# Optimization experiments

Hardware: AMD Instinct MI355X
Metric: run time of the kernel (lower is better)

Reference implementation:

```python
import jax, jax.numpy as jnp
import numpy as np

DIM = 512
HEADS = 8
HEAD_DIM = DIM // HEADS
SCALING = float(np.sqrt(HEAD_DIM))
B, S = 8, 2048


def setup_inputs() -> dict:
    key = jax.random.key(0)
    ks = jax.random.split(key, 6)
    x = jax.random.normal(ks[0], (B, S, DIM), dtype=jnp.float32)
    mask = jax.random.randint(ks[1], (B, S), 0, 2).astype(bool)
    mask = mask.at[:, 0].set(False)  # guarantee at least one unmasked key per row
    lim_qkv = 1.0 / np.sqrt(DIM)
    Wqkv = jax.random.uniform(ks[2], (3 * DIM, DIM), minval=-lim_qkv, maxval=lim_qkv, dtype=jnp.float32)
    bqkv = jax.random.uniform(ks[3], (3 * DIM,), minval=-lim_qkv, maxval=lim_qkv, dtype=jnp.float32)
    Wout = jax.random.uniform(ks[4], (DIM, DIM), minval=-lim_qkv, maxval=lim_qkv, dtype=jnp.float32)
    bout = jax.random.uniform(ks[5], (DIM,), minval=-lim_qkv, maxval=lim_qkv, dtype=jnp.float32)
    ln_g = jnp.ones((DIM,), dtype=jnp.float32)
    ln_b = jnp.zeros((DIM,), dtype=jnp.float32)
    return {"x": x, "mask": mask, "Wqkv": Wqkv, "bqkv": bqkv, "Wout": Wout, "bout": bout, "ln_g": ln_g, "ln_b": ln_b}


def reference(x, mask, Wqkv, bqkv, Wout, bout, ln_g, ln_b):
    b, s, _ = x.shape
    qkv = x @ Wqkv.T + bqkv                                   # [b, s, 3*dim]
    qkv = qkv.reshape(b, s, HEADS, HEAD_DIM, 3)               # torch reshape semantics (interleaved)
    q = qkv[..., 0]                                           # [b, s, h, d]
    k = qkv[..., 1]
    v = jax.nn.elu(qkv[..., 2])
    attn = jnp.einsum('bqhd,bkhd->bhqk', q, k) / SCALING      # [b, h, s, s]
    bias = jnp.where(mask[:, None, None, :], -jnp.inf, 0.0).astype(attn.dtype)
    attn = jax.nn.softmax(attn + bias, axis=-1)
    out = jnp.einsum('bhqk,bkhd->bqhd', attn, v).reshape(b, s, DIM)
    out = out @ Wout.T + bout
    mu = jnp.mean(out, axis=-1, keepdims=True)
    var = jnp.var(out, axis=-1, keepdims=True)
    out = (out - mu) / jnp.sqrt(var + 1e-5) * ln_g + ln_b
    return jax.nn.elu(out)
```

## Files before the change

### kernel.cpp

```cpp
#include <hip/hip_runtime.h>

#define DIM 512
#define HEADS 8
#define HD 64
#define NB 8
#define NS 2048
#define SCALE_INV 0.125f
#define C2F 0.18033688011112042f
#define NEG_BIG -1e30f
#define QSZ 8388608

typedef __attribute__((ext_vector_type(8))) short bf16x8;
typedef __attribute__((ext_vector_type(4))) float f32x4;

__device__ __forceinline__ float elu_f(float x) {
    return x > 0.0f ? x : (__expf(x) - 1.0f);
}
__device__ __forceinline__ short f2bf(float x) {
    union { float f; unsigned u; } v; v.f = x;
    unsigned r = v.u + 0x7FFFu + ((v.u >> 16) & 1u);
    return (short)(r >> 16);
}
__device__ __forceinline__ float exp2_hw(float x) {
    float r; asm("v_exp_f32 %0, %1" : "=v"(r) : "v"(x)); return r;
}
__device__ __forceinline__ unsigned cvt_pk_bf16(float a, float b) {
    unsigned r; asm("v_cvt_pk_bf16_f32 %0, %1, %2" : "=v"(r) : "v"(a), "v"(b)); return r;
}

__device__ __forceinline__ void gload16(const void* g, void* l) {
    __builtin_amdgcn_global_load_lds(
        (const __attribute__((address_space(1))) unsigned*)g,
        (__attribute__((address_space(3))) unsigned*)l, 16, 0, 0);
}
__device__ __forceinline__ void gload4(const void* g, void* l) {
    __builtin_amdgcn_global_load_lds(
        (const __attribute__((address_space(1))) unsigned*)g,
        (__attribute__((address_space(3))) unsigned*)l, 4, 0, 0);
}

#define X4 2097152
#define W14 196608
#define W24 65536
__global__ __launch_bounds__(256) void prep(
    const float* __restrict__ x, const float* __restrict__ Wqkv,
    const float* __restrict__ bqkv, const float* __restrict__ Wout,
    const int* __restrict__ mask,
    short* __restrict__ xb, short* __restrict__ Wp,
    float* __restrict__ bp, short* __restrict__ Wob,
    float* __restrict__ maskf)
{
    int i = blockIdx.x * 256 + threadIdx.x;
    if (i < X4) {
        float4 v = *(const float4*)(x + (size_t)i * 4);
        ushort4 o; o.x = (unsigned short)f2bf(v.x); o.y = (unsigned short)f2bf(v.y);
        o.z = (unsigned short)f2bf(v.z); o.w = (unsigned short)f2bf(v.w);
        *(ushort4*)(xb + (size_t)i * 4) = o;
    } else if (i < X4 + W14) {
        int j = i - X4;
        int np = j >> 7, k = (j & 127) * 4;
        int w = np >> 9, h = (np >> 6) & 7, d = np & 63;
        int n = h * 192 + d * 3 + w;
        float4 v = *(const float4*)(Wqkv + (size_t)n * 512 + k);
        ushort4 o; o.x = (unsigned short)f2bf(v.x); o.y = (unsigned short)f2bf(v.y);
        o.z = (unsigned short)f2bf(v.z); o.w = (unsigned short)f2bf(v.w);
        *(ushort4*)(Wp + (size_t)np * 512 + k) = o;
    } else if (i < X4 + W14 + W24) {
        int j = i - X4 - W14;
        float4 v = *(const float4*)(Wout + (size_t)j * 4);
        ushort4 o; o.x = (unsigned short)f2bf(v.x); o.y = (unsigned short)f2bf(v.y);
        o.z = (unsigned short)f2bf(v.z); o.w = (unsigned short)f2bf(v.w);
        *(ushort4*)(Wob + (size_t)j * 4) = o;
    } else if (i < X4 + W14 + W24 + 1536) {
        int j = i - X4 - W14 - W24;
        int w = j >> 9, h = (j >> 6) & 7, d = j & 63;
        bp[j] = bqkv[h * 192 + d * 3 + w];
    } else {
        int j = i - X4 - W14 - W24 - 1536;
        maskf[j] = mask[j] ? NEG_BIG : 0.0f;
    }
}

__global__ __launch_bounds__(256) void qkv_mfma(
    const short* __restrict__ A, const short* __restrict__ Bw,
    const float* __restrict__ bp, short* __restrict__ QKV)
{
    __shared__ short smem[2 * 128 * 64];
    short* As = smem;
    short* Bs = smem + 128 * 64;
    const int t = threadIdx.x, lane = t & 63, wv = t >> 6;
    const int c = lane & 15, quad = lane >> 4;
    const int wr = wv >> 1, wc = wv & 1;
    const int rsub = lane >> 3;
    const int csA = (lane & 7) ^ rsub;
    const int m0 = blockIdx.x * 128, n0 = blockIdx.y * 128;
    f32x4 acc[4][4];
    #pragma unroll
    for (int mi = 0; mi < 4; ++mi)
        #pragma unroll
        for (int nj = 0; nj < 4; ++nj)
            #pragma unroll
            for (int i = 0; i < 4; ++i) acc[mi][nj][i] = 0.0f;

    for (int k0 = 0; k0 < 512; k0 += 64) {
        if (k0) __syncthreads();
        #pragma unroll
        for (int p = 0; p < 4; ++p) {
            int r = p * 32 + wv * 8 + rsub;
            gload16(A  + (size_t)(m0 + r) * 512 + k0 + csA * 8, &As[(p * 4 + wv) * 512]);
            gload16(Bw + (size_t)(n0 + r) * 512 + k0 + csA * 8, &Bs[(p * 4 + wv) * 512]);
        }
        __syncthreads();
        bf16x8 af[4][2], bfr[4][2];
        #pragma unroll
        for (int mi = 0; mi < 4; ++mi) {
            int ar = wr * 64 + mi * 16 + c;
            af[mi][0] = *(const bf16x8*)&As[ar * 64 + ((quad       ^ (ar & 7)) * 8)];
            af[mi][1] = *(const bf16x8*)&As[ar * 64 + (((4 + quad) ^ (ar & 7)) * 8)];
        }
        #pragma unroll
        for (int nj = 0; nj < 4; ++nj) {
            int br = wc * 64 + nj * 16 + c;
            bfr[nj][0] = *(const bf16x8*)&Bs[br * 64 + ((quad       ^ (br & 7)) * 8)];
            bfr[nj][1] = *(const bf16x8*)&Bs[br * 64 + (((4 + quad) ^ (br & 7)) * 8)];
        }
        __builtin_amdgcn_s_setprio(1);
        #pragma unroll
        for (int mi = 0; mi < 4; ++mi)
            #pragma unroll
            for (int nj = 0; nj < 4; ++nj) {
                acc[mi][nj] = __builtin_amdgcn_mfma_f32_16x16x32_bf16(af[mi][0], bfr[nj][0], acc[mi][nj], 0, 0, 0);
                acc[mi][nj] = __builtin_amdgcn_mfma_f32_16x16x32_bf16(af[mi][1], bfr[nj][1], acc[mi][nj], 0, 0, 0);
            }
        __builtin_amdgcn_s_setprio(0);
    }

    const int w  = n0 >> 9;
    const int b  = m0 >> 11;
    const int hh = ((n0 + wc * 64) >> 6) & 7;
    float bv[4];
    #pragma unroll
    for (int nj = 0; nj < 4; ++nj) bv[nj] = bp[n0 + wc * 64 + nj * 16 + c];

    if (w < 2) {
        short* out = QKV + (size_t)w * QSZ + (size_t)(b * 8 + hh) * NS * 64;
        #pragma unroll
        for (int mi = 0; mi < 4; ++mi)
            #pragma unroll
            for (int i = 0; i < 4; ++i) {
                int s = (m0 & (NS - 1)) + wr * 64 + mi * 16 + quad * 4 + i;
                #pragma unroll
                for (int nj = 0; nj < 4; ++nj)
                    out[(size_t)s * 64 + nj * 16 + c] = f2bf(acc[mi][nj][i] + bv[nj]);
            }
    } else {
        __syncthreads();
        short* T = smem;
        #pragma unroll
        for (int mi = 0; mi < 4; ++mi)
            #pragma unroll
            for (int i = 0; i < 4; ++i) {
                int ml = wr * 64 + mi * 16 + quad * 4 + i;
                int mb = ml >> 3, mr = ml & 7;
                #pragma unroll
                for (int nj = 0; nj < 4; ++nj) {
                    int nl = wc * 64 + nj * 16 + c;
                    T[nl * 128 + ((mb ^ (nl & 15)) * 8) + mr] =
                        f2bf(elu_f(acc[mi][nj][i] + bv[nj]));
                }
            }
        __syncthreads();
        short* Vt = QKV + (size_t)2 * QSZ;
        #pragma unroll
        for (int p = 0; p < 8; ++p) {
            int idx = p * 256 + t, row = idx >> 4, ch = idx & 15;
            uint4 v = *(const uint4*)&T[row * 128 + ((ch ^ (row & 15)) * 8)];
            int d = row & 63;
            int h2 = ((n0 + row) >> 6) & 7;
            int sg = (m0 & (NS - 1)) + ch * 8;
            int kt = sg >> 6, ks = sg & 63;
            *(uint4*)(Vt + (((size_t)(b * 8 + h2) * 32 + kt) * 64 + d) * 64 + ks) = v;
        }
    }
}

__global__ __launch_bounds__(512, 4) void attn_mfma(
    const short* __restrict__ Qg, const short* __restrict__ Kg,
    const short* __restrict__ Vg, const float* __restrict__ maskf,
    short* __restrict__ O)
{
    __shared__ short Pt[128 * 64];
    __shared__ short Ks[2][64 * 64];
    __shared__ short Vs[2][64 * 64];
    __shared__ float msk[2][64];
    __shared__ float lw[128];

    const int t = threadIdx.x;
    const int lane = t & 63;
    const int wv = t >> 6;
    const int wq = wv & 3;
    const int wk = wv >> 2;
    const int c = lane & 15;
    const int quad = lane >> 4;
    const int bid = blockIdx.x;
    const int qt = bid & 15;
    const int h  = (bid >> 4) & 7;
    const int b  = bid >> 7;
    const int g  = b * 8 + h;
    const size_t base = (size_t)g * NS * HD;
    const int q0 = qt * 128;

    const int rsub = lane >> 3;
    const int csA  = (lane & 7) ^ rsub;
    const int csV  = ((lane & 7) - rsub) & 7;

    #pragma unroll
    for (int p = 0; p < 2; ++p) {
        int r = wv * 16 + p * 8 + rsub;
        gload16(Qg + base + (size_t)(q0 + r) * HD + csA * 8, &Pt[(wv * 2 + p) * 512]);
    }
    {
        int r = wv * 8 + rsub;
        gload16(Kg + base + (size_t)r * HD + csA * 8, &Ks[0][wv * 512]);
        gload16(Vg + (((size_t)g * 32 + 0) * 64 + r) * 64 + csV * 8, &Vs[0][wv * 512]);
        if (wv == 0) gload4(maskf + (size_t)b * NS + lane, &msk[0][0]);
    }
    __syncthreads();

    bf16x8 bq[2][2];
    #pragma unroll
    for (int nj = 0; nj < 2; ++nj) {
        int mq = wq * 32 + nj * 16 + c;
        bq[nj][0] = *(const bf16x8*)&Pt[mq * 64 + ((quad       ^ (mq & 7)) * 8)];
        bq[nj][1] = *(const bf16x8*)&Pt[mq * 64 + (((4 + quad) ^ (mq & 7)) * 8)];
    }
    __syncthreads();

    {
        int r = wv * 8 + rsub;
        gload16(Kg + base + (size_t)(64 + r) * HD + csA * 8, &Ks[1][wv * 512]);
        gload16(Vg + (((size_t)g * 32 + 1) * 64 + r) * 64 + csV * 8, &Vs[1][wv * 512]);
        if (wv == 0) gload4(maskf + (size_t)b * NS + 64 + lane, &msk[1][0]);
    }

    bf16x8 onesA;
    #pragma unroll
    for (int i = 0; i < 8; ++i) onesA[i] = (short)0x3F80;

    f32x4 o[4][2];
    #pragma unroll
    for (int dc = 0; dc < 4; ++dc)
        #pragma unroll
        for (int nj = 0; nj < 2; ++nj)
            #pragma unroll
            for (int i = 0; i < 4; ++i) o[dc][nj][i] = 0.0f;
    f32x4 lacc[2];
    #pragma unroll
    for (int nj = 0; nj < 2; ++nj)
        #pragma unroll
        for (int i = 0; i < 4; ++i) lacc[nj][i] = 0.0f;

    const int prot  = 8 * (c & 7);
    const int kbase = wk * 32;

    for (int kt = 0; kt < 32; ++kt) {
        const int cur = kt & 1;
        const short* Kc = Ks[cur];
        const short* Vc = Vs[cur];

        f32x4 st[2][2];
        __builtin_amdgcn_s_setprio(1);
        #pragma unroll
        for (int ks = 0; ks < 2; ++ks) {
            int kr = kbase + ks * 16 + c;
            bf16x8 ak0 = *(const bf16x8*)&Kc[kr * 64 + ((quad       ^ (kr & 7)) * 8)];
            bf16x8 ak1 = *(const bf16x8*)&Kc[kr * 64 + (((4 + quad) ^ (kr & 7)) * 8)];
            #pragma unroll
            for (int nj = 0; nj < 2; ++nj) {
                f32x4 a = {0.0f, 0.0f, 0.0f, 0.0f};
                a = __builtin_amdgcn_mfma_f32_16x16x32_bf16(ak0, bq[nj][0], a, 0, 0, 0);
                a = __builtin_amdgcn_mfma_f32_16x16x32_bf16(ak1, bq[nj][1], a, 0, 0, 0);
                st[ks][nj] = a;
            }
        }
        __builtin_amdgcn_s_setprio(0);

        #pragma unroll
        for (int ks = 0; ks < 2; ++ks) {
            float4 mb = *(const float4*)&msk[cur][kbase + ks * 16 + quad * 4];
            #pragma unroll
            for (int nj = 0; nj < 2; ++nj) {
                float p0 = exp2_hw(st[ks][nj][0] * C2F + mb.x);
                float p1 = exp2_hw(st[ks][nj][1] * C2F + mb.y);
                float p2 = exp2_hw(st[ks][nj][2] * C2F + mb.z);
                float p3 = exp2_hw(st[ks][nj][3] * C2F + mb.w);
                uint2 pk;
                pk.x = cvt_pk_bf16(p0, p1);
                pk.y = cvt_pk_bf16(p2, p3);
                *(uint2*)&Pt[(wq * 32 + nj * 16 + c) * 64 +
                             ((kbase + ks * 16 + quad * 4 + prot) & 63)] = pk;
            }
        }

        bf16x8 bp[2];
        #pragma unroll
        for (int nj = 0; nj < 2; ++nj)
            bp[nj] = *(const bf16x8*)&Pt[(wq * 32 + nj * 16 + c) * 64 +
                                         ((kbase + quad * 8 + prot) & 63)];

        __builtin_amdgcn_s_setprio(1);
        #pragma unroll
        for (int nj = 0; nj < 2; ++nj)
            lacc[nj] = __builtin_amdgcn_mfma_f32_16x16x32_bf16(onesA, bp[nj], lacc[nj], 0, 0, 0);
        #pragma unroll
        for (int dc = 0; dc < 4; ++dc) {
            int d = dc * 16 + c;
            int vrot = 8 * (d & 7);
            bf16x8 av = *(const bf16x8*)&Vc[d * 64 + ((kbase + quad * 8 + vrot) & 63)];
            #pragma unroll
            for (int nj = 0; nj < 2; ++nj)
                o[dc][nj] = __builtin_amdgcn_mfma_f32_16x16x32_bf16(av, bp[nj], o[dc][nj], 0, 0, 0);
        }
        __builtin_amdgcn_s_setprio(0);

        __syncthreads();

        if (kt + 2 < 32) {
            int r = wv * 8 + rsub;
            int k0n = (kt + 2) * 64;
            gload16(Kg + base + (size_t)(k0n + r) * HD + csA * 8, &Ks[cur][wv * 512]);
            gload16(Vg + (((size_t)g * 32 + (kt + 2)) * 64 + r) * 64 + csV * 8, &Vs[cur][wv * 512]);
            if (wv == 0) gload4(maskf + (size_t)b * NS + k0n + lane, &msk[cur][0]);
        }
    }

    float* rb = ((wq < 2) ? (float*)&Ks[0][0] : (float*)&Vs[0][0])
                + (wq & 1) * 2048 + lane * 32;
    if (wk == 1) {
        #pragma unroll
        for (int dc = 0; dc < 4; ++dc)
            #pragma unroll
            for (int nj = 0; nj < 2; ++nj)
                *(f32x4*)&rb[(((dc << 1) | nj) ^ (lane & 7)) << 2] = o[dc][nj];
        if (quad == 0) {
            lw[wq * 32 + c]      = lacc[0][0];
            lw[wq * 32 + 16 + c] = lacc[1][0];
        }
    }
    __syncthreads();
    if (wk == 0) {
        float l0 = lacc[0][0] + lw[wq * 32 + c];
        float l1 = lacc[1][0] + lw[wq * 32 + 16 + c];
        float inv0 = 1.0f / l0;
        float inv1 = 1.0f / l1;
        #pragma unroll
        for (int dc = 0; dc < 4; ++dc)
            #pragma unroll
            for (int nj = 0; nj < 2; ++nj)
                o[dc][nj] += *(const f32x4*)&rb[(((dc << 1) | nj) ^ (lane & 7)) << 2];
        #pragma unroll
        for (int nj = 0; nj < 2; ++nj) {
            float inv = nj ? inv1 : inv0;
            int q = q0 + wq * 32 + nj * 16 + c;
            short* orow = O + ((size_t)(b * NS + q)) * DIM + h * HD + quad * 4;
            #pragma unroll
            for (int dc = 0; dc < 4; ++dc) {
                uint2 pk;
                pk.x = (unsigned)(unsigned short)f2bf(o[dc][nj][0] * inv)
                     | ((unsigned)(unsigned short)f2bf(o[dc][nj][1] * inv) << 16);
                pk.y = (unsigned)(unsigned short)f2bf(o[dc][nj][2] * inv)
                     | ((unsigned)(unsigned short)f2bf(o[dc][nj][3] * inv) << 16);
                *(uint2*)(orow + dc * 16) = pk;
            }
        }
    }
}

__global__ __launch_bounds__(512) void out_ln(
    const short* __restrict__ A, const short* __restrict__ Bw,
    const float* __restrict__ bias, const float* __restrict__ g,
    const float* __restrict__ bt, float* __restrict__ out)
{
    __shared__ short As[64 * 64];
    __shared__ short Bs[512 * 64];
    const int t = threadIdx.x, lane = t & 63, wv = t >> 6;
    const int c = lane & 15, quad = lane >> 4;
    const int wr = wv >> 2, wc = wv & 3;
    const int rsub = lane >> 3;
    const int csA = (lane & 7) ^ rsub;
    const int m0 = blockIdx.x * 64;

    float bv[8], gg[8], bb[8];
    #pragma unroll
    for (int nj = 0; nj < 8; ++nj) {
        int col = wc * 128 + nj * 16 + c;
        bv[nj] = bias[col]; gg[nj] = g[col]; bb[nj] = bt[col];
    }

    f32x4 acc[2][8];
    #pragma unroll
    for (int mi = 0; mi < 2; ++mi)
        #pragma unroll
        for (int nj = 0; nj < 8; ++nj)
            #pragma unroll
            for (int i = 0; i < 4; ++i) acc[mi][nj][i] = 0.0f;

    for (int k0 = 0; k0 < 512; k0 += 64) {
        if (k0) __syncthreads();
        gload16(A + (size_t)(m0 + wv * 8 + rsub) * 512 + k0 + csA * 8, &As[wv * 512]);
        #pragma unroll
        for (int p = 0; p < 8; ++p) {
            int r = p * 64 + wv * 8 + rsub;
            gload16(Bw + (size_t)r * 512 + k0 + csA * 8, &Bs[(p * 8 + wv) * 512]);
        }
        __syncthreads();
        bf16x8 af[2][2];
        #pragma unroll
        for (int mi = 0; mi < 2; ++mi) {
            int ar = wr * 32 + mi * 16 + c;
            af[mi][0] = *(const bf16x8*)&As[ar * 64 + ((quad       ^ (ar & 7)) * 8)];
            af[mi][1] = *(const bf16x8*)&As[ar * 64 + (((4 + quad) ^ (ar & 7)) * 8)];
        }
        __builtin_amdgcn_s_setprio(1);
        #pragma unroll
        for (int nj = 0; nj < 8; ++nj) {
            int br = wc * 128 + nj * 16 + c;
            bf16x8 b0 = *(const bf16x8*)&Bs[br * 64 + ((quad       ^ (br & 7)) * 8)];
            bf16x8 b1 = *(const bf16x8*)&Bs[br * 64 + (((4 + quad) ^ (br & 7)) * 8)];
            #pragma unroll
            for (int mi = 0; mi < 2; ++mi) {
                acc[mi][nj] = __builtin_amdgcn_mfma_f32_16x16x32_bf16(af[mi][0], b0, acc[mi][nj], 0, 0, 0);
                acc[mi][nj] = __builtin_amdgcn_mfma_f32_16x16x32_bf16(af[mi][1], b1, acc[mi][nj], 0, 0, 0);
            }
        }
        __builtin_amdgcn_s_setprio(0);
    }
    __syncthreads();

    float* red = (float*)As;
    #pragma unroll
    for (int mi = 0; mi < 2; ++mi)
        #pragma unroll
        for (int i = 0; i < 4; ++i) {
            float s = 0.0f, ss = 0.0f;
            #pragma unroll
            for (int nj = 0; nj < 8; ++nj) {
                float z = acc[mi][nj][i] + bv[nj];
                s += z; ss += z * z;
            }
            s  += __shfl_xor(s, 1);  s  += __shfl_xor(s, 2);
            s  += __shfl_xor(s, 4);  s  += __shfl_xor(s, 8);
            ss += __shfl_xor(ss, 1); ss += __shfl_xor(ss, 2);
            ss += __shfl_xor(ss, 4); ss += __shfl_xor(ss, 8);
            if (c == 0) {
                int row = wr * 32 + mi * 16 + quad * 4 + i;
                red[wc * 64 + row]       = s;
                red[256 + wc * 64 + row] = ss;
            }
        }
    __syncthreads();
    #pragma unroll
    for (int mi = 0; mi < 2; ++mi)
        #pragma unroll
        for (int i = 0; i < 4; ++i) {
            int row = wr * 32 + mi * 16 + quad * 4 + i;
            float S1 = red[row] + red[64 + row] + red[128 + row] + red[192 + row];
            float S2 = red[256 + row] + red[320 + row] + red[384 + row] + red[448 + row];
            float mu   = S1 * (1.0f / DIM);
            float var  = S2 * (1.0f / DIM) - mu * mu;
            float rstd = rsqrtf(var + 1e-5f);
            float* orow = out + (size_t)(m0 + row) * DIM + wc * 128 + c;
            #pragma unroll
            for (int nj = 0; nj < 8; ++nj) {
                float z = acc[mi][nj][i] + bv[nj];
                orow[nj * 16] = elu_f((z - mu) * rstd * gg[nj] + bb[nj]);
            }
        }
}

extern "C" void kernel_launch(void* const* d_in, const int* in_sizes, int n_in,
                              void* d_out, int out_size, void* d_ws, size_t ws_size,
                              hipStream_t stream)
{
    const float* x    = (const float*)d_in[0];
    const int*   mask = (const int*)d_in[1];
    const float* Wqkv = (const float*)d_in[2];
    const float* bqkv = (const float*)d_in[3];
    const float* Wout = (const float*)d_in[4];
    const float* bout = (const float*)d_in[5];
    const float* ln_g = (const float*)d_in[6];
    const float* ln_b = (const float*)d_in[7];
    float* out = (float*)d_out;

    short* xb   = (short*)d_ws;
    short* Wp   = xb + QSZ;
    short* Wob  = Wp + 786432;
    short* QKV  = Wob + 262144;
    short* ATTb = QKV + 3 * (size_t)QSZ;
    float* bp   = (float*)(ATTb + QSZ);
    float* Zb   = bp + 1536;
    float* maskf = Zb + (size_t)QSZ - 16384;

    prep<<<9286, 256, 0, stream>>>(x, Wqkv, bqkv, Wout, mask, xb, Wp, bp, Wob, maskf);
    qkv_mfma<<<dim3(128, 12), 256, 0, stream>>>(xb, Wp, bp, QKV);
    attn_mfma<<<1024, 512, 0, stream>>>(QKV, QKV + QSZ, QKV + 2 * (size_t)QSZ, maskf, ATTb);
    out_ln<<<256, 512, 0, stream>>>(ATTb, Wob, bout, ln_g, ln_b, out);
}
```

Measured before the change: 245.5 us.

## Double-buffer LDS tiles in QKV and output-projection GEMM kernels

Both the QKV projection and the output-projection+LayerNorm GEMM kernels now keep two LDS buffers per operand. The tile for the next K step is prefetched into one buffer while MFMAs run on the other, so each step needs one barrier instead of two. The aim is to hide global-to-LDS load latency behind the matrix math. The cost is more shared memory: about 64KB for the QKV kernel and about 147KB for out_ln, which limits occupancy to a single block per CU for out_ln.

```diff
diff --git a/kernel.cpp b/kernel.cpp
--- a/kernel.cpp
+++ b/kernel.cpp
@@ -85,9 +85,7 @@
     const short* __restrict__ A, const short* __restrict__ Bw,
     const float* __restrict__ bp, short* __restrict__ QKV)
 {
-    __shared__ short smem[2 * 128 * 64];
-    short* As = smem;
-    short* Bs = smem + 128 * 64;
+    __shared__ short smem[4 * 128 * 64];
     const int t = threadIdx.x, lane = t & 63, wv = t >> 6;
     const int c = lane & 15, quad = lane >> 4;
     const int wr = wv >> 1, wc = wv & 1;
@@ -102,15 +100,30 @@
             #pragma unroll
             for (int i = 0; i < 4; ++i) acc[mi][nj][i] = 0.0f;
 
-    for (int k0 = 0; k0 < 512; k0 += 64) {
-        if (k0) __syncthreads();
-        #pragma unroll
-        for (int p = 0; p < 4; ++p) {
-            int r = p * 32 + wv * 8 + rsub;
-            gload16(A  + (size_t)(m0 + r) * 512 + k0 + csA * 8, &As[(p * 4 + wv) * 512]);
-            gload16(Bw + (size_t)(n0 + r) * 512 + k0 + csA * 8, &Bs[(p * 4 + wv) * 512]);
-        }
+    #pragma unroll
+    for (int p = 0; p < 4; ++p) {
+        int r = p * 32 + wv * 8 + rsub;
+        gload16(A  + (size_t)(m0 + r) * 512 + csA * 8, &smem[(p * 4 + wv) * 512]);
+        gload16(Bw + (size_t)(n0 + r) * 512 + csA * 8, &smem[8192 + (p * 4 + wv) * 512]);
+    }
+
+    #pragma unroll 2
+    for (int step = 0; step < 8; ++step) {
+        const int cur = step & 1;
         __syncthreads();
+        if (step < 7) {
+            int k0n = (step + 1) * 64;
+            #pragma unroll
+            for (int p = 0; p < 4; ++p) {
+                int r = p * 32 + wv * 8 + rsub;
+                gload16(A  + (size_t)(m0 + r) * 512 + k0n + csA * 8,
+                        &smem[(cur ^ 1) * 16384 + (p * 4 + wv) * 512]);
+                gload16(Bw + (size_t)(n0 + r) * 512 + k0n + csA * 8,
+                        &smem[(cur ^ 1) * 16384 + 8192 + (p * 4 + wv) * 512]);
+            }
+        }
+        const short* As = &smem[cur * 16384];
+        const short* Bs = &smem[cur * 16384 + 8192];
         bf16x8 af[4][2], bfr[4][2];
         #pragma unroll
         for (int mi = 0; mi < 4; ++mi) {
@@ -381,8 +394,8 @@
     const float* __restrict__ bias, const float* __restrict__ g,
     const float* __restrict__ bt, float* __restrict__ out)
 {
-    __shared__ short As[64 * 64];
-    __shared__ short Bs[512 * 64];
+    __shared__ short As[2][64 * 64];
+    __shared__ short Bs[2][512 * 64];
     const int t = threadIdx.x, lane = t & 63, wv = t >> 6;
     const int c = lane & 15, quad = lane >> 4;
     const int wr = wv >> 2, wc = wv & 3;
@@ -405,28 +418,41 @@
             #pragma unroll
             for (int i = 0; i < 4; ++i) acc[mi][nj][i] = 0.0f;
 
-    for (int k0 = 0; k0 < 512; k0 += 64) {
-        if (k0) __syncthreads();
-        gload16(A + (size_t)(m0 + wv * 8 + rsub) * 512 + k0 + csA * 8, &As[wv * 512]);
-        #pragma unroll
-        for (int p = 0; p < 8; ++p) {
-            int r = p * 64 + wv * 8 + rsub;
-            gload16(Bw + (size_t)r * 512 + k0 + csA * 8, &Bs[(p * 8 + wv) * 512]);
-        }
+    gload16(A + (size_t)(m0 + wv * 8 + rsub) * 512 + csA * 8, &As[0][wv * 512]);
+    #pragma unroll
+    for (int p = 0; p < 8; ++p) {
+        int r = p * 64 + wv * 8 + rsub;
+        gload16(Bw + (size_t)r * 512 + csA * 8, &Bs[0][(p * 8 + wv) * 512]);
+    }
+
+    #pragma unroll 2
+    for (int step = 0; step < 8; ++step) {
+        const int cur = step & 1;
         __syncthreads();
+        if (step < 7) {
+            int k0n = (step + 1) * 64;
+            gload16(A + (size_t)(m0 + wv * 8 + rsub) * 512 + k0n + csA * 8,
+                    &As[cur ^ 1][wv * 512]);
+            #pragma unroll
+            for (int p = 0; p < 8; ++p) {
+                int r = p * 64 + wv * 8 + rsub;
+                gload16(Bw + (size_t)r * 512 + k0n + csA * 8,
+                        &Bs[cur ^ 1][(p * 8 + wv) * 512]);
+            }
+        }
         bf16x8 af[2][2];
         #pragma unroll
         for (int mi = 0; mi < 2; ++mi) {
             int ar = wr * 32 + mi * 16 + c;
-            af[mi][0] = *(const bf16x8*)&As[ar * 64 + ((quad       ^ (ar & 7)) * 8)];
-            af[mi][1] = *(const bf16x8*)&As[ar * 64 + (((4 + quad) ^ (ar & 7)) * 8)];
+            af[mi][0] = *(const bf16x8*)&As[cur][ar * 64 + ((quad       ^ (ar & 7)) * 8)];
+            af[mi][1] = *(const bf16x8*)&As[cur][ar * 64 + (((4 + quad) ^ (ar & 7)) * 8)];
         }
         __builtin_amdgcn_s_setprio(1);
         #pragma unroll
         for (int nj = 0; nj < 8; ++nj) {
             int br = wc * 128 + nj * 16 + c;
-            bf16x8 b0 = *(const bf16x8*)&Bs[br * 64 + ((quad       ^ (br & 7)) * 8)];
-            bf16x8 b1 = *(const bf16x8*)&Bs[br * 64 + (((4 + quad) ^ (br & 7)) * 8)];
+            bf16x8 b0 = *(const bf16x8*)&Bs[cur][br * 64 + ((quad       ^ (br & 7)) * 8)];
+            bf16x8 b1 = *(const bf16x8*)&Bs[cur][br * 64 + (((4 + quad) ^ (br & 7)) * 8)];
             #pragma unroll
             for (int mi = 0; mi < 2; ++mi) {
                 acc[mi][nj] = __builtin_amdgcn_mfma_f32_16x16x32_bf16(af[mi][0], b0, acc[mi][nj], 0, 0, 0);
@@ -437,7 +463,7 @@
     }
     __syncthreads();
 
-    float* red = (float*)As;
+    float* red = (float*)&As[0][0];
     #pragma unroll
     for (int mi = 0; mi < 2; ++mi)
         #pragma unroll
```

New measurement: 235.1 us. 4.2% less time.
